# Kernel tuning notes

Hardware: AMD Instinct MI355X
Metric: run time of the kernel (lower is better)

The kernel has to match this reference:

```python
import jax, jax.numpy as jnp
import numpy as np

N_MEL = 80
N_CTX = 640  # n_text_channels + n_speaker_dim = 512 + 128
N_ATT = 128
TEMPERATURE = 1.0


def setup_inputs() -> dict:
    key = jax.random.key(0)
    ks = jax.random.split(key, 7)
    Tq, B, Tk = 512, 8, 256
    queries = jax.random.normal(ks[0], (Tq, B, N_MEL), dtype=jnp.float32)
    keys = jax.random.normal(ks[1], (Tk, B, N_CTX), dtype=jnp.float32)
    values = jax.random.normal(ks[2], (Tk, B, N_CTX), dtype=jnp.float32)
    # Linear weights (torch nn.Linear stores W as (out, in); y = x @ W.T)
    sq = 1.0 / np.sqrt(N_MEL)
    sk = 1.0 / np.sqrt(N_CTX)
    sv = 1.0 / np.sqrt(N_ATT)
    Wq = jax.random.normal(ks[3], (N_ATT, N_MEL), dtype=jnp.float32) * sq
    Wk = jax.random.normal(ks[4], (N_ATT, N_CTX), dtype=jnp.float32) * sk
    Wv = jax.random.normal(ks[5], (N_ATT, N_CTX), dtype=jnp.float32) * sk
    Wvec = jax.random.normal(ks[6], (N_ATT,), dtype=jnp.float32) * sv  # v: Linear(N_ATT, 1)
    return {"queries": queries, "keys": keys, "values": values,
            "Wq": Wq, "Wk": Wk, "Wv": Wv, "Wvec": Wvec}


def reference(queries, keys, values, Wq, Wk, Wv, Wvec):
    # Projections then time-major -> batch-major: (T,B,*) -> (B,T,C)
    q = jnp.einsum('tbi,ci->btc', queries, Wq)   # (B, Tq, C)
    k = jnp.einsum('tbi,ci->btc', keys, Wk)      # (B, Tk, C)
    v = jnp.einsum('tbi,ci->btc', values, Wv)    # (B, Tk, C)
    # Additive (Bahdanau) energies: broadcast add + tanh + v-dot reduce
    energy = jnp.tanh(q[:, :, None, :] + k[:, None, :, :])  # (B, Tq, Tk, C)
    attn = jnp.einsum('bqkc,c->bqk', energy, Wvec) / TEMPERATURE
    attn = jax.nn.softmax(attn, axis=2)          # softmax over Tk
    out = jnp.einsum('bqk,bkc->bqc', attn, v)    # (B, Tq, C)
    out = jnp.transpose(out, (0, 2, 1))          # (B, C, Tq)
    return (out, attn)
```

## Files before the change

### kernel.cpp

```cpp
#include <hip/hip_runtime.h>

#define TQ 512
#define TK 256
#define BB 8
#define CC 128

#define SCALE2L2E 2.8853900817779268f
#define L2E 1.4426950408889634f

__device__ __forceinline__ float fexp2(float x) { return __builtin_amdgcn_exp2f(x); }
__device__ __forceinline__ float frcp(float x)  { return __builtin_amdgcn_rcpf(x); }

typedef __fp16 h16x2 __attribute__((ext_vector_type(2)));
typedef __fp16 h16x4 __attribute__((ext_vector_type(4)));
typedef __fp16 h16x8 __attribute__((ext_vector_type(8)));
typedef _Float16 f16x8 __attribute__((ext_vector_type(8)));
typedef float f32x4 __attribute__((ext_vector_type(4)));

__device__ __forceinline__ f16x8 pack8(float4 lo, float4 hi) {
    h16x2 a0 = __builtin_amdgcn_cvt_pkrtz(lo.x, lo.y);
    h16x2 a1 = __builtin_amdgcn_cvt_pkrtz(lo.z, lo.w);
    h16x2 a2 = __builtin_amdgcn_cvt_pkrtz(hi.x, hi.y);
    h16x2 a3 = __builtin_amdgcn_cvt_pkrtz(hi.z, hi.w);
    h16x4 p0 = __builtin_shufflevector(a0, a1, 0, 1, 2, 3);
    h16x4 p1 = __builtin_shufflevector(a2, a3, 0, 1, 2, 3);
    h16x8 r = __builtin_shufflevector(p0, p1, 0, 1, 2, 3, 4, 5, 6, 7);
    return __builtin_bit_cast(f16x8, r);
}

__device__ __forceinline__ h16x4 pack4h(float4 v) {
    h16x2 lo = __builtin_amdgcn_cvt_pkrtz(v.x, v.y);
    h16x2 hi = __builtin_amdgcn_cvt_pkrtz(v.z, v.w);
    return __builtin_shufflevector(lo, hi, 0, 1, 2, 3);
}

#define CWK 10240
#define CWV 10240
#define CWQ 1536
#define CXQ 49152
#define CXK 163840
#define CXV 163840
#define CTOT (CWK + CWV + CWQ + CXQ + CXK + CXV)

__global__ __launch_bounds__(256) void convert_kernel(
    const float* __restrict__ Wk, const float* __restrict__ Wv,
    const float* __restrict__ Wq, const float* __restrict__ q_in,
    const float* __restrict__ k_in, const float* __restrict__ v_in,
    f16x8* __restrict__ Wk16s, f16x8* __restrict__ Wv16s,
    f16x8* __restrict__ Wq16s, f16x8* __restrict__ Xq16s,
    f16x8* __restrict__ Xk16s, f16x8* __restrict__ Xv16s)
{
    const int d = blockIdx.x * 256 + threadIdx.x;
    if (d >= CTOT) return;
    const f16x8 zero = {};

    const float* __restrict__ src;
    f16x8* __restrict__ dst;
    int dd, K;
    if (d < CWK)                         { dd = d; src = Wk; dst = Wk16s; K = 640; }
    else if (d < CWK + CWV)              { dd = d - CWK; src = Wv; dst = Wv16s; K = 640; }
    else if (d < CWK + CWV + CWQ)        { dd = d - CWK - CWV; src = Wq; dst = Wq16s; K = 80; }
    else if (d < CWK + CWV + CWQ + CXQ)  { dd = d - CWK - CWV - CWQ; src = q_in; dst = Xq16s; K = 80; }
    else if (d < CTOT - CXV)             { dd = d - CWK - CWV - CWQ - CXQ; src = k_in; dst = Xk16s; K = 640; }
    else                                 { dd = d - (CTOT - CXV); src = v_in; dst = Xv16s; K = 640; }

    const int nstep = (K == 640) ? 20 : 3;
    const int per = nstep * 64;
    const int tile = dd / per, rem = dd % per;
    const int s = rem >> 6, l = rem & 63;
    const int lr = l & 15, lk = l >> 4;
    const int r = tile * 16 + lr, k0 = s * 32 + lk * 8;
    if (K == 80 && k0 >= 80) { dst[dd] = zero; return; }
    float4 lo = *(const float4*)&src[(size_t)r * K + k0];
    float4 hi = *(const float4*)&src[(size_t)r * K + k0 + 4];
    dst[dd] = pack8(lo, hi);
}

__global__ __launch_bounds__(256) void proj_mfma(
    const _Float16* __restrict__ Wk16s, const _Float16* __restrict__ Wv16s,
    const _Float16* __restrict__ Wq16s, const _Float16* __restrict__ Xq16s,
    const _Float16* __restrict__ Xk16s, const _Float16* __restrict__ Xv16s,
    float* __restrict__ eqp, float* __restrict__ ekp, _Float16* __restrict__ v16s)
{
    const int tid = threadIdx.x;
    const int w = tid >> 6;
    const int l = tid & 63;
    const int lr = l & 15, lk = l >> 4;
    const int id = blockIdx.x;
    const int j = (id >> 1) * 4 + w;

    f32x4 acc0 = {0.f, 0.f, 0.f, 0.f};
    f32x4 acc1 = {0.f, 0.f, 0.f, 0.f};

    if ((id & 1) == 0) {
        const int tensor = j >> 9;
        const int jj = j & 511;
        const int rtile = jj >> 2;
        const int c0 = (jj & 3) * 32;
        const int r0 = rtile * 16;
        const _Float16* __restrict__ Xs = tensor ? Xv16s : Xk16s;
        const _Float16* __restrict__ Wt = tensor ? Wv16s : Wk16s;

        const _Float16* __restrict__ A0 = Xs + (size_t)rtile * 10240 + l * 8;
        const _Float16* __restrict__ B0 = Wt + (c0 >> 4) * 10240 + l * 8;
        const _Float16* __restrict__ B1 = B0 + 10240;

#pragma unroll
        for (int s = 0; s < 20; ++s) {
            f16x8 a = *(const f16x8*)(A0 + s * 512);
            f16x8 b0 = *(const f16x8*)(B0 + s * 512);
            f16x8 b1 = *(const f16x8*)(B1 + s * 512);
            acc0 = __builtin_amdgcn_mfma_f32_16x16x32_f16(a, b0, acc0, 0, 0, 0);
            acc1 = __builtin_amdgcn_mfma_f32_16x16x32_f16(a, b1, acc1, 0, 0, 0);
        }

        if (tensor == 0) {
#pragma unroll
            for (int jr = 0; jr < 4; ++jr) {
                int r = r0 + lk * 4 + jr;
                int t = r >> 3, bt = r & 7;
                ekp[((size_t)bt * CC + c0 + lr) * TK + t] = fexp2(SCALE2L2E * acc0[jr]);
                ekp[((size_t)bt * CC + c0 + 16 + lr) * TK + t] = fexp2(SCALE2L2E * acc1[jr]);
            }
        } else {
#pragma unroll
            for (int jr = 0; jr < 4; ++jr) {
                int r = r0 + lk * 4 + jr;
                int t = r >> 3, bt = r & 7;
                int base = bt * 32768 + (t >> 5) * 512 + ((t >> 3) & 3) * 128
                         + lr * 8 + (t & 7);
                v16s[base + (c0 >> 4) * 4096] = (_Float16)acc0[jr];
                v16s[base + ((c0 >> 4) + 1) * 4096] = (_Float16)acc1[jr];
            }
        }
    } else {
        const int rtile = j >> 2;
        const int c0 = (j & 3) * 32;

        const _Float16* __restrict__ A0 = Xq16s + (size_t)rtile * 1536 + l * 8;
        const _Float16* __restrict__ B0 = Wq16s + (c0 >> 4) * 1536 + l * 8;
        const _Float16* __restrict__ B1 = B0 + 1536;

#pragma unroll
        for (int s = 0; s < 3; ++s) {
            f16x8 a = *(const f16x8*)(A0 + s * 512);
            f16x8 bb0 = *(const f16x8*)(B0 + s * 512);
            f16x8 bb1 = *(const f16x8*)(B1 + s * 512);
            acc0 = __builtin_amdgcn_mfma_f32_16x16x32_f16(a, bb0, acc0, 0, 0, 0);
            acc1 = __builtin_amdgcn_mfma_f32_16x16x32_f16(a, bb1, acc1, 0, 0, 0);
        }

#pragma unroll
        for (int jr = 0; jr < 4; ++jr) {
            int r = rtile * 16 + lk * 4 + jr;
            int t = r >> 3, bt = r & 7;
            eqp[((size_t)bt * TQ + t) * CC + c0 + lr] = fexp2(SCALE2L2E * acc0[jr]);
            eqp[((size_t)bt * TQ + t) * CC + c0 + 16 + lr] = fexp2(SCALE2L2E * acc1[jr]);
        }
    }
}

__global__ __launch_bounds__(512, 2) void attn_pv_kernel(
    const float* __restrict__ eqp, const float* __restrict__ ekp,
    const float* __restrict__ Wvec, const _Float16* __restrict__ v16s,
    float* __restrict__ attn_out, float* __restrict__ out)
{
    __shared__ float pa[4][64][17];
    __shared__ _Float16 pl[16][264];

    const int tid = threadIdx.x;
    const int lane = tid & 63;
    const int w = __builtin_amdgcn_readfirstlane(tid >> 6);
    const int g = w >> 1;
    const int h = w & 1;
    const int b = blockIdx.y;
    const int q0g = blockIdx.x * 16;
    const int q0 = q0g + g * 4;

    const float* __restrict__ qr0 = eqp + ((size_t)b * TQ + q0) * CC + h * 64;
    const float* __restrict__ qr1 = qr0 + CC;
    const float* __restrict__ qr2 = qr1 + CC;
    const float* __restrict__ qr3 = qr2 + CC;
    const float* __restrict__ kb = ekp + (size_t)b * CC * TK + (h * 64) * TK + lane * 4;
    const float* __restrict__ wvp = Wvec + h * 64;

    float sw = Wvec[lane] + Wvec[64 + lane];
#pragma unroll
    for (int m = 32; m >= 1; m >>= 1) sw += __shfl_xor(sw, m, 64);

    float a0[4] = {0.f, 0.f, 0.f, 0.f};
    float a1[4] = {0.f, 0.f, 0.f, 0.f};
    float a2[4] = {0.f, 0.f, 0.f, 0.f};
    float a3[4] = {0.f, 0.f, 0.f, 0.f};

    float4 k0 = *(const float4*)&kb[0 * TK];
    float4 k1 = *(const float4*)&kb[1 * TK];
    float4 k2 = *(const float4*)&kb[2 * TK];
    float4 k3 = *(const float4*)&kb[3 * TK];
    float4 wv = *(const float4*)&wvp[0];
    float4 qa = *(const float4*)&qr0[0];
    float4 qb = *(const float4*)&qr1[0];
    float4 qc = *(const float4*)&qr2[0];
    float4 qd = *(const float4*)&qr3[0];

    for (int c4 = 0; c4 < 64; c4 += 4) {
        float4 n0, n1, n2, n3, nwv, nqa, nqb, nqc, nqd;
        if (c4 + 4 < 64) {
            n0 = *(const float4*)&kb[(c4 + 4) * TK];
            n1 = *(const float4*)&kb[(c4 + 5) * TK];
            n2 = *(const float4*)&kb[(c4 + 6) * TK];
            n3 = *(const float4*)&kb[(c4 + 7) * TK];
            nwv = *(const float4*)&wvp[c4 + 4];
            nqa = *(const float4*)&qr0[c4 + 4];
            nqb = *(const float4*)&qr1[c4 + 4];
            nqc = *(const float4*)&qr2[c4 + 4];
            nqd = *(const float4*)&qr3[c4 + 4];
        }
#define CCOMP(KF, WW, EA, EB, EC, ED)                                   \
        a0[0] = fmaf(WW, frcp(fmaf(EA, KF.x, 1.f)), a0[0]);             \
        a0[1] = fmaf(WW, frcp(fmaf(EA, KF.y, 1.f)), a0[1]);             \
        a0[2] = fmaf(WW, frcp(fmaf(EA, KF.z, 1.f)), a0[2]);             \
        a0[3] = fmaf(WW, frcp(fmaf(EA, KF.w, 1.f)), a0[3]);             \
        a1[0] = fmaf(WW, frcp(fmaf(EB, KF.x, 1.f)), a1[0]);             \
        a1[1] = fmaf(WW, frcp(fmaf(EB, KF.y, 1.f)), a1[1]);             \
        a1[2] = fmaf(WW, frcp(fmaf(EB, KF.z, 1.f)), a1[2]);             \
        a1[3] = fmaf(WW, frcp(fmaf(EB, KF.w, 1.f)), a1[3]);             \
        a2[0] = fmaf(WW, frcp(fmaf(EC, KF.x, 1.f)), a2[0]);             \
        a2[1] = fmaf(WW, frcp(fmaf(EC, KF.y, 1.f)), a2[1]);             \
        a2[2] = fmaf(WW, frcp(fmaf(EC, KF.z, 1.f)), a2[2]);             \
        a2[3] = fmaf(WW, frcp(fmaf(EC, KF.w, 1.f)), a2[3]);             \
        a3[0] = fmaf(WW, frcp(fmaf(ED, KF.x, 1.f)), a3[0]);             \
        a3[1] = fmaf(WW, frcp(fmaf(ED, KF.y, 1.f)), a3[1]);             \
        a3[2] = fmaf(WW, frcp(fmaf(ED, KF.z, 1.f)), a3[2]);             \
        a3[3] = fmaf(WW, frcp(fmaf(ED, KF.w, 1.f)), a3[3]);
        CCOMP(k0, wv.x, qa.x, qb.x, qc.x, qd.x)
        CCOMP(k1, wv.y, qa.y, qb.y, qc.y, qd.y)
        CCOMP(k2, wv.z, qa.z, qb.z, qc.z, qd.z)
        CCOMP(k3, wv.w, qa.w, qb.w, qc.w, qd.w)
#undef CCOMP
        k0 = n0; k1 = n1; k2 = n2; k3 = n3;
        wv = nwv; qa = nqa; qb = nqb; qc = nqc; qd = nqd;
    }

    if (h == 1) {
#pragma unroll
        for (int jj = 0; jj < 4; ++jj) {
            pa[g][lane][jj]      = a0[jj];
            pa[g][lane][4 + jj]  = a1[jj];
            pa[g][lane][8 + jj]  = a2[jj];
            pa[g][lane][12 + jj] = a3[jj];
        }
    }
    __syncthreads();

    if (h == 0) {
#pragma unroll
        for (int jj = 0; jj < 4; ++jj) {
            a0[jj] += pa[g][lane][jj];
            a1[jj] += pa[g][lane][4 + jj];
            a2[jj] += pa[g][lane][8 + jj];
            a3[jj] += pa[g][lane][12 + jj];
        }

        float sc0[4], sc1[4], sc2[4], sc3[4];
#pragma unroll
        for (int j = 0; j < 4; ++j) {
            sc0[j] = sw - 2.f * a0[j];
            sc1[j] = sw - 2.f * a1[j];
            sc2[j] = sw - 2.f * a2[j];
            sc3[j] = sw - 2.f * a3[j];
        }

        float m0 = fmaxf(fmaxf(sc0[0], sc0[1]), fmaxf(sc0[2], sc0[3]));
        float m1 = fmaxf(fmaxf(sc1[0], sc1[1]), fmaxf(sc1[2], sc1[3]));
        float m2 = fmaxf(fmaxf(sc2[0], sc2[1]), fmaxf(sc2[2], sc2[3]));
        float m3 = fmaxf(fmaxf(sc3[0], sc3[1]), fmaxf(sc3[2], sc3[3]));
#pragma unroll
        for (int m = 32; m >= 1; m >>= 1) {
            m0 = fmaxf(m0, __shfl_xor(m0, m, 64));
            m1 = fmaxf(m1, __shfl_xor(m1, m, 64));
            m2 = fmaxf(m2, __shfl_xor(m2, m, 64));
            m3 = fmaxf(m3, __shfl_xor(m3, m, 64));
        }
        float e0[4], e1[4], e2[4], e3[4];
        float s0 = 0.f, s1 = 0.f, s2 = 0.f, s3 = 0.f;
#pragma unroll
        for (int j = 0; j < 4; ++j) {
            e0[j] = fexp2((sc0[j] - m0) * L2E); s0 += e0[j];
            e1[j] = fexp2((sc1[j] - m1) * L2E); s1 += e1[j];
            e2[j] = fexp2((sc2[j] - m2) * L2E); s2 += e2[j];
            e3[j] = fexp2((sc3[j] - m3) * L2E); s3 += e3[j];
        }
#pragma unroll
        for (int m = 32; m >= 1; m >>= 1) {
            s0 += __shfl_xor(s0, m, 64);
            s1 += __shfl_xor(s1, m, 64);
            s2 += __shfl_xor(s2, m, 64);
            s3 += __shfl_xor(s3, m, 64);
        }
        const float r0 = frcp(s0), r1 = frcp(s1), r2 = frcp(s2), r3 = frcp(s3);

        const float4 p0 = make_float4(e0[0] * r0, e0[1] * r0, e0[2] * r0, e0[3] * r0);
        const float4 p1 = make_float4(e1[0] * r1, e1[1] * r1, e1[2] * r1, e1[3] * r1);
        const float4 p2 = make_float4(e2[0] * r2, e2[1] * r2, e2[2] * r2, e2[3] * r2);
        const float4 p3 = make_float4(e3[0] * r3, e3[1] * r3, e3[2] * r3, e3[3] * r3);

        float* __restrict__ po = attn_out + ((size_t)b * TQ + q0) * TK + lane * 4;
        *(float4*)(po + 0 * TK) = p0;
        *(float4*)(po + 1 * TK) = p1;
        *(float4*)(po + 2 * TK) = p2;
        *(float4*)(po + 3 * TK) = p3;

        *(h16x4*)&pl[g * 4 + 0][lane * 4] = pack4h(p0);
        *(h16x4*)&pl[g * 4 + 1][lane * 4] = pack4h(p1);
        *(h16x4*)&pl[g * 4 + 2][lane * 4] = pack4h(p2);
        *(h16x4*)&pl[g * 4 + 3][lane * 4] = pack4h(p3);
    }
    __syncthreads();

    const int lr = lane & 15, lk = lane >> 4;
    const _Float16* __restrict__ Vr = v16s + b * 32768 + w * 4096 + lane * 8;
    f32x4 acc = {0.f, 0.f, 0.f, 0.f};
#pragma unroll
    for (int s = 0; s < 8; ++s) {
        f16x8 a = *(const f16x8*)&pl[lr][s * 32 + lk * 8];
        f16x8 bv = *(const f16x8*)(Vr + s * 512);
        acc = __builtin_amdgcn_mfma_f32_16x16x32_f16(a, bv, acc, 0, 0, 0);
    }
    float4 o = make_float4(acc[0], acc[1], acc[2], acc[3]);
    *(float4*)&out[((size_t)b * CC + w * 16 + lr) * TQ + q0g + lk * 4] = o;
}

extern "C" void kernel_launch(void* const* d_in, const int* in_sizes, int n_in,
                              void* d_out, int out_size, void* d_ws, size_t ws_size,
                              hipStream_t stream) {
    const float* queries = (const float*)d_in[0];
    const float* keys    = (const float*)d_in[1];
    const float* values  = (const float*)d_in[2];
    const float* Wq      = (const float*)d_in[3];
    const float* Wk      = (const float*)d_in[4];
    const float* Wv      = (const float*)d_in[5];
    const float* Wvec    = (const float*)d_in[6];

    float* out  = (float*)d_out;
    float* attn = out + BB * CC * TQ;

    float* ws = (float*)d_ws;
    float* eqp = ws;
    float* ekp = eqp + 4096 * CC;
    _Float16* v16s = (_Float16*)(ekp + 2048 * CC);
    _Float16* Wk16s = v16s + 8 * 32768;
    _Float16* Wv16s = Wk16s + 81920;
    _Float16* Wq16s = Wv16s + 81920;
    _Float16* Xq16s = Wq16s + 12288;
    _Float16* Xk16s = Xq16s + 393216;
    _Float16* Xv16s = Xk16s + 1310720;

    convert_kernel<<<dim3((CTOT + 255) / 256), 256, 0, stream>>>(
        Wk, Wv, Wq, queries, keys, values,
        (f16x8*)Wk16s, (f16x8*)Wv16s, (f16x8*)Wq16s,
        (f16x8*)Xq16s, (f16x8*)Xk16s, (f16x8*)Xv16s);
    proj_mfma<<<dim3(512), 256, 0, stream>>>(
        Wk16s, Wv16s, Wq16s, Xq16s, Xk16s, Xv16s, eqp, ekp, v16s);
    attn_pv_kernel<<<dim3(32, 8), 512, 0, stream>>>(
        eqp, ekp, Wvec, v16s, attn, out);
}
```

Baseline: 40.93 us.

## Fuse convert, projection and attention kernels into one persistent kernel with grid barriers

Merges the three kernel launches into a single 256-block persistent kernel. The conversion phase becomes a grid-stride loop, and the projection and attention phases are remapped onto block and wave ids, with software grid barriers (atomic counter plus spin) between them. The aim is to remove the launch gaps and tail effects between kernels. In exchange it adds a memset launch and barrier spin cost, and it relies on all 256 blocks being co-resident to avoid deadlock.

```diff
diff --git a/kernel.cpp b/kernel.cpp
--- a/kernel.cpp
+++ b/kernel.cpp
@@ -42,293 +42,310 @@
 #define CXV 163840
 #define CTOT (CWK + CWV + CWQ + CXQ + CXK + CXV)
 
-__global__ __launch_bounds__(256) void convert_kernel(
+#define NBLK 256
+#define NTHR 512
+
+__device__ __forceinline__ void gbarrier(unsigned* cnt, unsigned target) {
+    __syncthreads();
+    if (threadIdx.x == 0) {
+        __threadfence();
+        atomicAdd(cnt, 1u);
+        while (__hip_atomic_load(cnt, __ATOMIC_ACQUIRE,
+                                 __HIP_MEMORY_SCOPE_AGENT) < target) {
+            __builtin_amdgcn_s_sleep(2);
+        }
+    }
+    __syncthreads();
+}
+
+__global__ __launch_bounds__(NTHR, 2) void fused_kernel(
+    const float* __restrict__ q_in, const float* __restrict__ k_in,
+    const float* __restrict__ v_in, const float* __restrict__ Wq,
     const float* __restrict__ Wk, const float* __restrict__ Wv,
-    const float* __restrict__ Wq, const float* __restrict__ q_in,
-    const float* __restrict__ k_in, const float* __restrict__ v_in,
-    f16x8* __restrict__ Wk16s, f16x8* __restrict__ Wv16s,
-    f16x8* __restrict__ Wq16s, f16x8* __restrict__ Xq16s,
-    f16x8* __restrict__ Xk16s, f16x8* __restrict__ Xv16s)
+    const float* __restrict__ Wvec, float* __restrict__ out,
+    float* __restrict__ attn_out, float* __restrict__ wsbase,
+    unsigned* __restrict__ bar)
 {
-    const int d = blockIdx.x * 256 + threadIdx.x;
-    if (d >= CTOT) return;
-    const f16x8 zero = {};
-
-    const float* __restrict__ src;
-    f16x8* __restrict__ dst;
-    int dd, K;
-    if (d < CWK)                         { dd = d; src = Wk; dst = Wk16s; K = 640; }
-    else if (d < CWK + CWV)              { dd = d - CWK; src = Wv; dst = Wv16s; K = 640; }
-    else if (d < CWK + CWV + CWQ)        { dd = d - CWK - CWV; src = Wq; dst = Wq16s; K = 80; }
-    else if (d < CWK + CWV + CWQ + CXQ)  { dd = d - CWK - CWV - CWQ; src = q_in; dst = Xq16s; K = 80; }
-    else if (d < CTOT - CXV)             { dd = d - CWK - CWV - CWQ - CXQ; src = k_in; dst = Xk16s; K = 640; }
-    else                                 { dd = d - (CTOT - CXV); src = v_in; dst = Xv16s; K = 640; }
-
-    const int nstep = (K == 640) ? 20 : 3;
-    const int per = nstep * 64;
-    const int tile = dd / per, rem = dd % per;
-    const int s = rem >> 6, l = rem & 63;
-    const int lr = l & 15, lk = l >> 4;
-    const int r = tile * 16 + lr, k0 = s * 32 + lk * 8;
-    if (K == 80 && k0 >= 80) { dst[dd] = zero; return; }
-    float4 lo = *(const float4*)&src[(size_t)r * K + k0];
-    float4 hi = *(const float4*)&src[(size_t)r * K + k0 + 4];
-    dst[dd] = pack8(lo, hi);
-}
-
-__global__ __launch_bounds__(256) void proj_mfma(
-    const _Float16* __restrict__ Wk16s, const _Float16* __restrict__ Wv16s,
-    const _Float16* __restrict__ Wq16s, const _Float16* __restrict__ Xq16s,
-    const _Float16* __restrict__ Xk16s, const _Float16* __restrict__ Xv16s,
-    float* __restrict__ eqp, float* __restrict__ ekp, _Float16* __restrict__ v16s)
-{
-    const int tid = threadIdx.x;
-    const int w = tid >> 6;
-    const int l = tid & 63;
-    const int lr = l & 15, lk = l >> 4;
-    const int id = blockIdx.x;
-    const int j = (id >> 1) * 4 + w;
-
-    f32x4 acc0 = {0.f, 0.f, 0.f, 0.f};
-    f32x4 acc1 = {0.f, 0.f, 0.f, 0.f};
-
-    if ((id & 1) == 0) {
-        const int tensor = j >> 9;
-        const int jj = j & 511;
-        const int rtile = jj >> 2;
-        const int c0 = (jj & 3) * 32;
-        const int r0 = rtile * 16;
-        const _Float16* __restrict__ Xs = tensor ? Xv16s : Xk16s;
-        const _Float16* __restrict__ Wt = tensor ? Wv16s : Wk16s;
-
-        const _Float16* __restrict__ A0 = Xs + (size_t)rtile * 10240 + l * 8;
-        const _Float16* __restrict__ B0 = Wt + (c0 >> 4) * 10240 + l * 8;
-        const _Float16* __restrict__ B1 = B0 + 10240;
-
-#pragma unroll
-        for (int s = 0; s < 20; ++s) {
-            f16x8 a = *(const f16x8*)(A0 + s * 512);
-            f16x8 b0 = *(const f16x8*)(B0 + s * 512);
-            f16x8 b1 = *(const f16x8*)(B1 + s * 512);
-            acc0 = __builtin_amdgcn_mfma_f32_16x16x32_f16(a, b0, acc0, 0, 0, 0);
-            acc1 = __builtin_amdgcn_mfma_f32_16x16x32_f16(a, b1, acc1, 0, 0, 0);
-        }
-
-        if (tensor == 0) {
-#pragma unroll
-            for (int jr = 0; jr < 4; ++jr) {
-                int r = r0 + lk * 4 + jr;
-                int t = r >> 3, bt = r & 7;
-                ekp[((size_t)bt * CC + c0 + lr) * TK + t] = fexp2(SCALE2L2E * acc0[jr]);
-                ekp[((size_t)bt * CC + c0 + 16 + lr) * TK + t] = fexp2(SCALE2L2E * acc1[jr]);
-            }
-        } else {
-#pragma unroll
-            for (int jr = 0; jr < 4; ++jr) {
-                int r = r0 + lk * 4 + jr;
-                int t = r >> 3, bt = r & 7;
-                int base = bt * 32768 + (t >> 5) * 512 + ((t >> 3) & 3) * 128
-                         + lr * 8 + (t & 7);
-                v16s[base + (c0 >> 4) * 4096] = (_Float16)acc0[jr];
-                v16s[base + ((c0 >> 4) + 1) * 4096] = (_Float16)acc1[jr];
-            }
-        }
-    } else {
-        const int rtile = j >> 2;
-        const int c0 = (j & 3) * 32;
-
-        const _Float16* __restrict__ A0 = Xq16s + (size_t)rtile * 1536 + l * 8;
-        const _Float16* __restrict__ B0 = Wq16s + (c0 >> 4) * 1536 + l * 8;
-        const _Float16* __restrict__ B1 = B0 + 1536;
-
-#pragma unroll
-        for (int s = 0; s < 3; ++s) {
-            f16x8 a = *(const f16x8*)(A0 + s * 512);
-            f16x8 bb0 = *(const f16x8*)(B0 + s * 512);
-            f16x8 bb1 = *(const f16x8*)(B1 + s * 512);
-            acc0 = __builtin_amdgcn_mfma_f32_16x16x32_f16(a, bb0, acc0, 0, 0, 0);
-            acc1 = __builtin_amdgcn_mfma_f32_16x16x32_f16(a, bb1, acc1, 0, 0, 0);
-        }
-
-#pragma unroll
-        for (int jr = 0; jr < 4; ++jr) {
-            int r = rtile * 16 + lk * 4 + jr;
-            int t = r >> 3, bt = r & 7;
-            eqp[((size_t)bt * TQ + t) * CC + c0 + lr] = fexp2(SCALE2L2E * acc0[jr]);
-            eqp[((size_t)bt * TQ + t) * CC + c0 + 16 + lr] = fexp2(SCALE2L2E * acc1[jr]);
-        }
-    }
-}
-
-__global__ __launch_bounds__(512, 2) void attn_pv_kernel(
-    const float* __restrict__ eqp, const float* __restrict__ ekp,
-    const float* __restrict__ Wvec, const _Float16* __restrict__ v16s,
-    float* __restrict__ attn_out, float* __restrict__ out)
-{
+    float* eqp = wsbase;
+    float* ekp = eqp + 4096 * CC;
+    _Float16* v16s = (_Float16*)(ekp + 2048 * CC);
+    _Float16* Wk16s = v16s + 8 * 32768;
+    _Float16* Wv16s = Wk16s + 81920;
+    _Float16* Wq16s = Wv16s + 81920;
+    _Float16* Xq16s = Wq16s + 12288;
+    _Float16* Xk16s = Xq16s + 393216;
+    _Float16* Xv16s = Xk16s + 1310720;
+
     __shared__ float pa[4][64][17];
     __shared__ _Float16 pl[16][264];
 
     const int tid = threadIdx.x;
+    const int bid = blockIdx.x;
+    const int w = __builtin_amdgcn_readfirstlane(tid >> 6);
     const int lane = tid & 63;
-    const int w = __builtin_amdgcn_readfirstlane(tid >> 6);
-    const int g = w >> 1;
-    const int h = w & 1;
-    const int b = blockIdx.y;
-    const int q0g = blockIdx.x * 16;
-    const int q0 = q0g + g * 4;
-
-    const float* __restrict__ qr0 = eqp + ((size_t)b * TQ + q0) * CC + h * 64;
-    const float* __restrict__ qr1 = qr0 + CC;
-    const float* __restrict__ qr2 = qr1 + CC;
-    const float* __restrict__ qr3 = qr2 + CC;
-    const float* __restrict__ kb = ekp + (size_t)b * CC * TK + (h * 64) * TK + lane * 4;
-    const float* __restrict__ wvp = Wvec + h * 64;
-
-    float sw = Wvec[lane] + Wvec[64 + lane];
-#pragma unroll
-    for (int m = 32; m >= 1; m >>= 1) sw += __shfl_xor(sw, m, 64);
-
-    float a0[4] = {0.f, 0.f, 0.f, 0.f};
-    float a1[4] = {0.f, 0.f, 0.f, 0.f};
-    float a2[4] = {0.f, 0.f, 0.f, 0.f};
-    float a3[4] = {0.f, 0.f, 0.f, 0.f};
-
-    float4 k0 = *(const float4*)&kb[0 * TK];
-    float4 k1 = *(const float4*)&kb[1 * TK];
-    float4 k2 = *(const float4*)&kb[2 * TK];
-    float4 k3 = *(const float4*)&kb[3 * TK];
-    float4 wv = *(const float4*)&wvp[0];
-    float4 qa = *(const float4*)&qr0[0];
-    float4 qb = *(const float4*)&qr1[0];
-    float4 qc = *(const float4*)&qr2[0];
-    float4 qd = *(const float4*)&qr3[0];
-
-    for (int c4 = 0; c4 < 64; c4 += 4) {
-        float4 n0, n1, n2, n3, nwv, nqa, nqb, nqc, nqd;
-        if (c4 + 4 < 64) {
-            n0 = *(const float4*)&kb[(c4 + 4) * TK];
-            n1 = *(const float4*)&kb[(c4 + 5) * TK];
-            n2 = *(const float4*)&kb[(c4 + 6) * TK];
-            n3 = *(const float4*)&kb[(c4 + 7) * TK];
-            nwv = *(const float4*)&wvp[c4 + 4];
-            nqa = *(const float4*)&qr0[c4 + 4];
-            nqb = *(const float4*)&qr1[c4 + 4];
-            nqc = *(const float4*)&qr2[c4 + 4];
-            nqd = *(const float4*)&qr3[c4 + 4];
-        }
+
+    for (int d = bid * NTHR + tid; d < CTOT; d += NBLK * NTHR) {
+        const f16x8 zero = {};
+        const float* __restrict__ src;
+        f16x8* __restrict__ dst;
+        int dd, K;
+        if (d < CWK)                         { dd = d; src = Wk; dst = (f16x8*)Wk16s; K = 640; }
+        else if (d < CWK + CWV)              { dd = d - CWK; src = Wv; dst = (f16x8*)Wv16s; K = 640; }
+        else if (d < CWK + CWV + CWQ)        { dd = d - CWK - CWV; src = Wq; dst = (f16x8*)Wq16s; K = 80; }
+        else if (d < CWK + CWV + CWQ + CXQ)  { dd = d - CWK - CWV - CWQ; src = q_in; dst = (f16x8*)Xq16s; K = 80; }
+        else if (d < CTOT - CXV)             { dd = d - CWK - CWV - CWQ - CXQ; src = k_in; dst = (f16x8*)Xk16s; K = 640; }
+        else                                 { dd = d - (CTOT - CXV); src = v_in; dst = (f16x8*)Xv16s; K = 640; }
+
+        const int nstep = (K == 640) ? 20 : 3;
+        const int per = nstep * 64;
+        const int tile = dd / per, rem = dd % per;
+        const int s = rem >> 6, l = rem & 63;
+        const int lr2 = l & 15, lk2 = l >> 4;
+        const int r = tile * 16 + lr2, k0 = s * 32 + lk2 * 8;
+        if (K == 80 && k0 >= 80) { dst[dd] = zero; continue; }
+        float4 lo = *(const float4*)&src[(size_t)r * K + k0];
+        float4 hi = *(const float4*)&src[(size_t)r * K + k0 + 4];
+        dst[dd] = pack8(lo, hi);
+    }
+    gbarrier(&bar[0], NBLK);
+
+    {
+        const int lr = lane & 15, lk = lane >> 4;
+        const int wg = bid * 8 + w;
+        const int j = wg >> 1;
+
+        f32x4 acc0 = {0.f, 0.f, 0.f, 0.f};
+        f32x4 acc1 = {0.f, 0.f, 0.f, 0.f};
+
+        if ((wg & 1) == 0) {
+            const int tensor = j >> 9;
+            const int jj = j & 511;
+            const int rtile = jj >> 2;
+            const int c0 = (jj & 3) * 32;
+            const int r0 = rtile * 16;
+            const _Float16* __restrict__ Xs = tensor ? Xv16s : Xk16s;
+            const _Float16* __restrict__ Wt = tensor ? Wv16s : Wk16s;
+
+            const _Float16* __restrict__ A0 = Xs + (size_t)rtile * 10240 + lane * 8;
+            const _Float16* __restrict__ B0 = Wt + (c0 >> 4) * 10240 + lane * 8;
+            const _Float16* __restrict__ B1 = B0 + 10240;
+
+#pragma unroll
+            for (int s = 0; s < 20; ++s) {
+                f16x8 a = *(const f16x8*)(A0 + s * 512);
+                f16x8 b0 = *(const f16x8*)(B0 + s * 512);
+                f16x8 b1 = *(const f16x8*)(B1 + s * 512);
+                acc0 = __builtin_amdgcn_mfma_f32_16x16x32_f16(a, b0, acc0, 0, 0, 0);
+                acc1 = __builtin_amdgcn_mfma_f32_16x16x32_f16(a, b1, acc1, 0, 0, 0);
+            }
+
+            if (tensor == 0) {
+#pragma unroll
+                for (int jr = 0; jr < 4; ++jr) {
+                    int r = r0 + lk * 4 + jr;
+                    int t = r >> 3, bt = r & 7;
+                    ekp[((size_t)bt * CC + c0 + lr) * TK + t] = fexp2(SCALE2L2E * acc0[jr]);
+                    ekp[((size_t)bt * CC + c0 + 16 + lr) * TK + t] = fexp2(SCALE2L2E * acc1[jr]);
+                }
+            } else {
+#pragma unroll
+                for (int jr = 0; jr < 4; ++jr) {
+                    int r = r0 + lk * 4 + jr;
+                    int t = r >> 3, bt = r & 7;
+                    int base = bt * 32768 + (t >> 5) * 512 + ((t >> 3) & 3) * 128
+                             + lr * 8 + (t & 7);
+                    v16s[base + (c0 >> 4) * 4096] = (_Float16)acc0[jr];
+                    v16s[base + ((c0 >> 4) + 1) * 4096] = (_Float16)acc1[jr];
+                }
+            }
+        } else {
+            const int rtile = j >> 2;
+            const int c0 = (j & 3) * 32;
+
+            const _Float16* __restrict__ A0 = Xq16s + (size_t)rtile * 1536 + lane * 8;
+            const _Float16* __restrict__ B0 = Wq16s + (c0 >> 4) * 1536 + lane * 8;
+            const _Float16* __restrict__ B1 = B0 + 1536;
+
+#pragma unroll
+            for (int s = 0; s < 3; ++s) {
+                f16x8 a = *(const f16x8*)(A0 + s * 512);
+                f16x8 bb0 = *(const f16x8*)(B0 + s * 512);
+                f16x8 bb1 = *(const f16x8*)(B1 + s * 512);
+                acc0 = __builtin_amdgcn_mfma_f32_16x16x32_f16(a, bb0, acc0, 0, 0, 0);
+                acc1 = __builtin_amdgcn_mfma_f32_16x16x32_f16(a, bb1, acc1, 0, 0, 0);
+            }
+
+#pragma unroll
+            for (int jr = 0; jr < 4; ++jr) {
+                int r = rtile * 16 + lk * 4 + jr;
+                int t = r >> 3, bt = r & 7;
+                eqp[((size_t)bt * TQ + t) * CC + c0 + lr] = fexp2(SCALE2L2E * acc0[jr]);
+                eqp[((size_t)bt * TQ + t) * CC + c0 + 16 + lr] = fexp2(SCALE2L2E * acc1[jr]);
+            }
+        }
+    }
+    gbarrier(&bar[1], NBLK);
+
+    {
+        const int g = w >> 1;
+        const int h = w & 1;
+        const int b = bid >> 5;
+        const int q0g = (bid & 31) * 16;
+        const int q0 = q0g + g * 4;
+
+        const float* __restrict__ qr0 = eqp + ((size_t)b * TQ + q0) * CC + h * 64;
+        const float* __restrict__ qr1 = qr0 + CC;
+        const float* __restrict__ qr2 = qr1 + CC;
+        const float* __restrict__ qr3 = qr2 + CC;
+        const float* __restrict__ kb = ekp + (size_t)b * CC * TK + (h * 64) * TK + lane * 4;
+        const float* __restrict__ wvp = Wvec + h * 64;
+
+        float sw = Wvec[lane] + Wvec[64 + lane];
+#pragma unroll
+        for (int m = 32; m >= 1; m >>= 1) sw += __shfl_xor(sw, m, 64);
+
+        float a0[4] = {0.f, 0.f, 0.f, 0.f};
+        float a1[4] = {0.f, 0.f, 0.f, 0.f};
+        float a2[4] = {0.f, 0.f, 0.f, 0.f};
+        float a3[4] = {0.f, 0.f, 0.f, 0.f};
+
+        float4 k0 = *(const float4*)&kb[0 * TK];
+        float4 k1 = *(const float4*)&kb[1 * TK];
+        float4 k2 = *(const float4*)&kb[2 * TK];
+        float4 k3 = *(const float4*)&kb[3 * TK];
+        float4 wv = *(const float4*)&wvp[0];
+        float4 qa = *(const float4*)&qr0[0];
+        float4 qb = *(const float4*)&qr1[0];
+        float4 qc = *(const float4*)&qr2[0];
+        float4 qd = *(const float4*)&qr3[0];
+
+        for (int c4 = 0; c4 < 64; c4 += 4) {
+            float4 n0, n1, n2, n3, nwv, nqa, nqb, nqc, nqd;
+            if (c4 + 4 < 64) {
+                n0 = *(const float4*)&kb[(c4 + 4) * TK];
+                n1 = *(const float4*)&kb[(c4 + 5) * TK];
+                n2 = *(const float4*)&kb[(c4 + 6) * TK];
+                n3 = *(const float4*)&kb[(c4 + 7) * TK];
+                nwv = *(const float4*)&wvp[c4 + 4];
+                nqa = *(const float4*)&qr0[c4 + 4];
+                nqb = *(const float4*)&qr1[c4 + 4];
+                nqc = *(const float4*)&qr2[c4 + 4];
+                nqd = *(const float4*)&qr3[c4 + 4];
+            }
 #define CCOMP(KF, WW, EA, EB, EC, ED)                                   \
-        a0[0] = fmaf(WW, frcp(fmaf(EA, KF.x, 1.f)), a0[0]);             \
-        a0[1] = fmaf(WW, frcp(fmaf(EA, KF.y, 1.f)), a0[1]);             \
-        a0[2] = fmaf(WW, frcp(fmaf(EA, KF.z, 1.f)), a0[2]);             \
-        a0[3] = fmaf(WW, frcp(fmaf(EA, KF.w, 1.f)), a0[3]);             \
-        a1[0] = fmaf(WW, frcp(fmaf(EB, KF.x, 1.f)), a1[0]);             \
-        a1[1] = fmaf(WW, frcp(fmaf(EB, KF.y, 1.f)), a1[1]);             \
-        a1[2] = fmaf(WW, frcp(fmaf(EB, KF.z, 1.f)), a1[2]);             \
-        a1[3] = fmaf(WW, frcp(fmaf(EB, KF.w, 1.f)), a1[3]);             \
-        a2[0] = fmaf(WW, frcp(fmaf(EC, KF.x, 1.f)), a2[0]);             \
-        a2[1] = fmaf(WW, frcp(fmaf(EC, KF.y, 1.f)), a2[1]);             \
-        a2[2] = fmaf(WW, frcp(fmaf(EC, KF.z, 1.f)), a2[2]);             \
-        a2[3] = fmaf(WW, frcp(fmaf(EC, KF.w, 1.f)), a2[3]);             \
-        a3[0] = fmaf(WW, frcp(fmaf(ED, KF.x, 1.f)), a3[0]);             \
-        a3[1] = fmaf(WW, frcp(fmaf(ED, KF.y, 1.f)), a3[1]);             \
-        a3[2] = fmaf(WW, frcp(fmaf(ED, KF.z, 1.f)), a3[2]);             \
-        a3[3] = fmaf(WW, frcp(fmaf(ED, KF.w, 1.f)), a3[3]);
-        CCOMP(k0, wv.x, qa.x, qb.x, qc.x, qd.x)
-        CCOMP(k1, wv.y, qa.y, qb.y, qc.y, qd.y)
-        CCOMP(k2, wv.z, qa.z, qb.z, qc.z, qd.z)
-        CCOMP(k3, wv.w, qa.w, qb.w, qc.w, qd.w)
+            a0[0] = fmaf(WW, frcp(fmaf(EA, KF.x, 1.f)), a0[0]);         \
+            a0[1] = fmaf(WW, frcp(fmaf(EA, KF.y, 1.f)), a0[1]);         \
+            a0[2] = fmaf(WW, frcp(fmaf(EA, KF.z, 1.f)), a0[2]);         \
+            a0[3] = fmaf(WW, frcp(fmaf(EA, KF.w, 1.f)), a0[3]);         \
+            a1[0] = fmaf(WW, frcp(fmaf(EB, KF.x, 1.f)), a1[0]);         \
+            a1[1] = fmaf(WW, frcp(fmaf(EB, KF.y, 1.f)), a1[1]);         \
+            a1[2] = fmaf(WW, frcp(fmaf(EB, KF.z, 1.f)), a1[2]);         \
+            a1[3] = fmaf(WW, frcp(fmaf(EB, KF.w, 1.f)), a1[3]);         \
+            a2[0] = fmaf(WW, frcp(fmaf(EC, KF.x, 1.f)), a2[0]);         \
+            a2[1] = fmaf(WW, frcp(fmaf(EC, KF.y, 1.f)), a2[1]);         \
+            a2[2] = fmaf(WW, frcp(fmaf(EC, KF.z, 1.f)), a2[2]);         \
+            a2[3] = fmaf(WW, frcp(fmaf(EC, KF.w, 1.f)), a2[3]);         \
+            a3[0] = fmaf(WW, frcp(fmaf(ED, KF.x, 1.f)), a3[0]);         \
+            a3[1] = fmaf(WW, frcp(fmaf(ED, KF.y, 1.f)), a3[1]);         \
+            a3[2] = fmaf(WW, frcp(fmaf(ED, KF.z, 1.f)), a3[2]);         \
+            a3[3] = fmaf(WW, frcp(fmaf(ED, KF.w, 1.f)), a3[3]);
+            CCOMP(k0, wv.x, qa.x, qb.x, qc.x, qd.x)
+            CCOMP(k1, wv.y, qa.y, qb.y, qc.y, qd.y)
+            CCOMP(k2, wv.z, qa.z, qb.z, qc.z, qd.z)
+            CCOMP(k3, wv.w, qa.w, qb.w, qc.w, qd.w)
 #undef CCOMP
-        k0 = n0; k1 = n1; k2 = n2; k3 = n3;
-        wv = nwv; qa = nqa; qb = nqb; qc = nqc; qd = nqd;
+            k0 = n0; k1 = n1; k2 = n2; k3 = n3;
+            wv = nwv; qa = nqa; qb = nqb; qc = nqc; qd = nqd;
+        }
+
+        if (h == 1) {
+#pragma unroll
+            for (int jj = 0; jj < 4; ++jj) {
+                pa[g][lane][jj]      = a0[jj];
+                pa[g][lane][4 + jj]  = a1[jj];
+                pa[g][lane][8 + jj]  = a2[jj];
+                pa[g][lane][12 + jj] = a3[jj];
+            }
+        }
+        __syncthreads();
+
+        if (h == 0) {
+#pragma unroll
+            for (int jj = 0; jj < 4; ++jj) {
+                a0[jj] += pa[g][lane][jj];
+                a1[jj] += pa[g][lane][4 + jj];
+                a2[jj] += pa[g][lane][8 + jj];
+                a3[jj] += pa[g][lane][12 + jj];
+            }
+
+            float sc0[4], sc1[4], sc2[4], sc3[4];
+#pragma unroll
+            for (int j = 0; j < 4; ++j) {
+                sc0[j] = sw - 2.f * a0[j];
+                sc1[j] = sw - 2.f * a1[j];
+                sc2[j] = sw - 2.f * a2[j];
+                sc3[j] = sw - 2.f * a3[j];
+            }
+
+            float m0 = fmaxf(fmaxf(sc0[0], sc0[1]), fmaxf(sc0[2], sc0[3]));
+            float m1 = fmaxf(fmaxf(sc1[0], sc1[1]), fmaxf(sc1[2], sc1[3]));
+            float m2 = fmaxf(fmaxf(sc2[0], sc2[1]), fmaxf(sc2[2], sc2[3]));
+            float m3 = fmaxf(fmaxf(sc3[0], sc3[1]), fmaxf(sc3[2], sc3[3]));
+#pragma unroll
+            for (int m = 32; m >= 1; m >>= 1) {
+                m0 = fmaxf(m0, __shfl_xor(m0, m, 64));
+                m1 = fmaxf(m1, __shfl_xor(m1, m, 64));
+                m2 = fmaxf(m2, __shfl_xor(m2, m, 64));
+                m3 = fmaxf(m3, __shfl_xor(m3, m, 64));
+            }
+            float e0[4], e1[4], e2[4], e3[4];
+            float s0 = 0.f, s1 = 0.f, s2 = 0.f, s3 = 0.f;
+#pragma unroll
+            for (int j = 0; j < 4; ++j) {
+                e0[j] = fexp2((sc0[j] - m0) * L2E); s0 += e0[j];
+                e1[j] = fexp2((sc1[j] - m1) * L2E); s1 += e1[j];
+                e2[j] = fexp2((sc2[j] - m2) * L2E); s2 += e2[j];
+                e3[j] = fexp2((sc3[j] - m3) * L2E); s3 += e3[j];
+            }
+#pragma unroll
+            for (int m = 32; m >= 1; m >>= 1) {
+                s0 += __shfl_xor(s0, m, 64);
+                s1 += __shfl_xor(s1, m, 64);
+                s2 += __shfl_xor(s2, m, 64);
+                s3 += __shfl_xor(s3, m, 64);
+            }
+            const float r0 = frcp(s0), r1 = frcp(s1), r2 = frcp(s2), r3 = frcp(s3);
+
+            const float4 p0 = make_float4(e0[0] * r0, e0[1] * r0, e0[2] * r0, e0[3] * r0);
+            const float4 p1 = make_float4(e1[0] * r1, e1[1] * r1, e1[2] * r1, e1[3] * r1);
+            const float4 p2 = make_float4(e2[0] * r2, e2[1] * r2, e2[2] * r2, e2[3] * r2);
+            const float4 p3 = make_float4(e3[0] * r3, e3[1] * r3, e3[2] * r3, e3[3] * r3);
+
+            float* __restrict__ po = attn_out + ((size_t)b * TQ + q0) * TK + lane * 4;
+            *(float4*)(po + 0 * TK) = p0;
+            *(float4*)(po + 1 * TK) = p1;
+            *(float4*)(po + 2 * TK) = p2;
+            *(float4*)(po + 3 * TK) = p3;
+
+            *(h16x4*)&pl[g * 4 + 0][lane * 4] = pack4h(p0);
+            *(h16x4*)&pl[g * 4 + 1][lane * 4] = pack4h(p1);
+            *(h16x4*)&pl[g * 4 + 2][lane * 4] = pack4h(p2);
+            *(h16x4*)&pl[g * 4 + 3][lane * 4] = pack4h(p3);
+        }
+        __syncthreads();
+
+        const int lr = lane & 15, lk = lane >> 4;
+        const _Float16* __restrict__ Vr = v16s + b * 32768 + w * 4096 + lane * 8;
+        f32x4 acc = {0.f, 0.f, 0.f, 0.f};
+#pragma unroll
+        for (int s = 0; s < 8; ++s) {
+            f16x8 a = *(const f16x8*)&pl[lr][s * 32 + lk * 8];
+            f16x8 bv = *(const f16x8*)(Vr + s * 512);
+            acc = __builtin_amdgcn_mfma_f32_16x16x32_f16(a, bv, acc, 0, 0, 0);
+        }
+        float4 o = make_float4(acc[0], acc[1], acc[2], acc[3]);
+        *(float4*)&out[((size_t)b * CC + w * 16 + lr) * TQ + q0g + lk * 4] = o;
     }
-
-    if (h == 1) {
-#pragma unroll
-        for (int jj = 0; jj < 4; ++jj) {
-            pa[g][lane][jj]      = a0[jj];
-            pa[g][lane][4 + jj]  = a1[jj];
-            pa[g][lane][8 + jj]  = a2[jj];
-            pa[g][lane][12 + jj] = a3[jj];
-        }
-    }
-    __syncthreads();
-
-    if (h == 0) {
-#pragma unroll
-        for (int jj = 0; jj < 4; ++jj) {
-            a0[jj] += pa[g][lane][jj];
-            a1[jj] += pa[g][lane][4 + jj];
-            a2[jj] += pa[g][lane][8 + jj];
-            a3[jj] += pa[g][lane][12 + jj];
-        }
-
-        float sc0[4], sc1[4], sc2[4], sc3[4];
-#pragma unroll
-        for (int j = 0; j < 4; ++j) {
-            sc0[j] = sw - 2.f * a0[j];
-            sc1[j] = sw - 2.f * a1[j];
-            sc2[j] = sw - 2.f * a2[j];
-            sc3[j] = sw - 2.f * a3[j];
-        }
-
-        float m0 = fmaxf(fmaxf(sc0[0], sc0[1]), fmaxf(sc0[2], sc0[3]));
-        float m1 = fmaxf(fmaxf(sc1[0], sc1[1]), fmaxf(sc1[2], sc1[3]));
-        float m2 = fmaxf(fmaxf(sc2[0], sc2[1]), fmaxf(sc2[2], sc2[3]));
-        float m3 = fmaxf(fmaxf(sc3[0], sc3[1]), fmaxf(sc3[2], sc3[3]));
-#pragma unroll
-        for (int m = 32; m >= 1; m >>= 1) {
-            m0 = fmaxf(m0, __shfl_xor(m0, m, 64));
-            m1 = fmaxf(m1, __shfl_xor(m1, m, 64));
-            m2 = fmaxf(m2, __shfl_xor(m2, m, 64));
-            m3 = fmaxf(m3, __shfl_xor(m3, m, 64));
-        }
-        float e0[4], e1[4], e2[4], e3[4];
-        float s0 = 0.f, s1 = 0.f, s2 = 0.f, s3 = 0.f;
-#pragma unroll
-        for (int j = 0; j < 4; ++j) {
-            e0[j] = fexp2((sc0[j] - m0) * L2E); s0 += e0[j];
-            e1[j] = fexp2((sc1[j] - m1) * L2E); s1 += e1[j];
-            e2[j] = fexp2((sc2[j] - m2) * L2E); s2 += e2[j];
-            e3[j] = fexp2((sc3[j] - m3) * L2E); s3 += e3[j];
-        }
-#pragma unroll
-        for (int m = 32; m >= 1; m >>= 1) {
-            s0 += __shfl_xor(s0, m, 64);
-            s1 += __shfl_xor(s1, m, 64);
-            s2 += __shfl_xor(s2, m, 64);
-            s3 += __shfl_xor(s3, m, 64);
-        }
-        const float r0 = frcp(s0), r1 = frcp(s1), r2 = frcp(s2), r3 = frcp(s3);
-
-        const float4 p0 = make_float4(e0[0] * r0, e0[1] * r0, e0[2] * r0, e0[3] * r0);
-        const float4 p1 = make_float4(e1[0] * r1, e1[1] * r1, e1[2] * r1, e1[3] * r1);
-        const float4 p2 = make_float4(e2[0] * r2, e2[1] * r2, e2[2] * r2, e2[3] * r2);
-        const float4 p3 = make_float4(e3[0] * r3, e3[1] * r3, e3[2] * r3, e3[3] * r3);
-
-        float* __restrict__ po = attn_out + ((size_t)b * TQ + q0) * TK + lane * 4;
-        *(float4*)(po + 0 * TK) = p0;
-        *(float4*)(po + 1 * TK) = p1;
-        *(float4*)(po + 2 * TK) = p2;
-        *(float4*)(po + 3 * TK) = p3;
-
-        *(h16x4*)&pl[g * 4 + 0][lane * 4] = pack4h(p0);
-        *(h16x4*)&pl[g * 4 + 1][lane * 4] = pack4h(p1);
-        *(h16x4*)&pl[g * 4 + 2][lane * 4] = pack4h(p2);
-        *(h16x4*)&pl[g * 4 + 3][lane * 4] = pack4h(p3);
-    }
-    __syncthreads();
-
-    const int lr = lane & 15, lk = lane >> 4;
-    const _Float16* __restrict__ Vr = v16s + b * 32768 + w * 4096 + lane * 8;
-    f32x4 acc = {0.f, 0.f, 0.f, 0.f};
-#pragma unroll
-    for (int s = 0; s < 8; ++s) {
-        f16x8 a = *(const f16x8*)&pl[lr][s * 32 + lk * 8];
-        f16x8 bv = *(const f16x8*)(Vr + s * 512);
-        acc = __builtin_amdgcn_mfma_f32_16x16x32_f16(a, bv, acc, 0, 0, 0);
-    }
-    float4 o = make_float4(acc[0], acc[1], acc[2], acc[3]);
-    *(float4*)&out[((size_t)b * CC + w * 16 + lr) * TQ + q0g + lk * 4] = o;
 }
 
 extern "C" void kernel_launch(void* const* d_in, const int* in_sizes, int n_in,
@@ -344,24 +361,14 @@
 
     float* out  = (float*)d_out;
     float* attn = out + BB * CC * TQ;
-
-    float* ws = (float*)d_ws;
-    float* eqp = ws;
-    float* ekp = eqp + 4096 * CC;
-    _Float16* v16s = (_Float16*)(ekp + 2048 * CC);
-    _Float16* Wk16s = v16s + 8 * 32768;
-    _Float16* Wv16s = Wk16s + 81920;
-    _Float16* Wq16s = Wv16s + 81920;
-    _Float16* Xq16s = Wq16s + 12288;
-    _Float16* Xk16s = Xq16s + 393216;
-    _Float16* Xv16s = Xk16s + 1310720;
-
-    convert_kernel<<<dim3((CTOT + 255) / 256), 256, 0, stream>>>(
-        Wk, Wv, Wq, queries, keys, values,
-        (f16x8*)Wk16s, (f16x8*)Wv16s, (f16x8*)Wq16s,
-        (f16x8*)Xq16s, (f16x8*)Xk16s, (f16x8*)Xv16s);
-    proj_mfma<<<dim3(512), 256, 0, stream>>>(
-        Wk16s, Wv16s, Wq16s, Xq16s, Xk16s, Xv16s, eqp, ekp, v16s);
-    attn_pv_kernel<<<dim3(32, 8), 512, 0, stream>>>(
-        eqp, ekp, Wvec, v16s, attn, out);
-}
+    float* wsf  = (float*)d_ws;
+
+    size_t ws_floats = (size_t)4096 * CC + 2048 * CC
+                     + (8 * 32768 + 81920 + 81920 + 12288 + 393216
+                        + 1310720 + 1310720) / 2;
+    unsigned* bar = (unsigned*)(wsf + ws_floats);
+
+    hipMemsetAsync(bar, 0, 2 * sizeof(unsigned), stream);
+    fused_kernel<<<dim3(NBLK), dim3(NTHR), 0, stream>>>(
+        queries, keys, values, Wq, Wk, Wv, Wvec, out, attn, wsf, bar);
+}
```

New measurement: 85.87 us. +109.8%, slower.
